# Performance work log

Hardware: AMD Instinct MI355X
Metric: run time of the kernel (lower is better)

The kernel has to match this reference:

```python
import jax, jax.numpy as jnp
import numpy as np

EPS = 1e-5  # torch BatchNorm1d default eps


def setup_inputs() -> dict:
    key = jax.random.key(0)
    ks = jax.random.split(key, 8)
    B, H, D, DO = 8192, 8, 512, 256
    return {
        "x_concepts_encoded": jax.random.normal(ks[0], (B, H, D), dtype=jnp.float32),
        "relevance_weights": jax.random.uniform(ks[1], (B, H), dtype=jnp.float32),
        "bn_gamma": jax.random.uniform(ks[2], (D,), dtype=jnp.float32) + 0.5,
        "bn_beta": jax.random.normal(ks[3], (D,), dtype=jnp.float32) * 0.1,
        "bn_mean": jax.random.normal(ks[4], (D,), dtype=jnp.float32) * 0.1,
        "bn_var": jax.random.uniform(ks[5], (D,), dtype=jnp.float32) + 0.5,
        "W": jax.random.normal(ks[6], (DO, D), dtype=jnp.float32) / np.sqrt(D),
        "b": jax.random.normal(ks[7], (DO,), dtype=jnp.float32) * 0.01,
    }


def reference(x_concepts_encoded, relevance_weights, bn_gamma, bn_beta, bn_mean, bn_var, W, b):
    B, H = relevance_weights.shape
    x = x_concepts_encoded.reshape(B * H, -1)            # [B*H, D]
    # BatchNorm1d (inference: running stats) fused as scale/shift
    inv = bn_gamma * jax.lax.rsqrt(bn_var + EPS)
    h = x * inv + (bn_beta - bn_mean * inv)              # [B*H, D]
    # Swish
    h = h * jax.nn.sigmoid(h)
    # Linear
    out = h @ W.T + b                                    # [B*H, DO]
    # relevance-weighted sum over heads
    out = jnp.einsum('bhd,bh->bd', out.reshape(B, H, -1), relevance_weights)
    return out
```

## Files before the change

kernel.cpp:

```cpp
#include <hip/hip_runtime.h>
#include <hip/hip_bf16.h>

#define NB 8192
#define NH 8
#define ND 512
#define NO 256
#define ROWS 16
#define TPB 512

typedef __attribute__((ext_vector_type(8))) short short8;
typedef __attribute__((ext_vector_type(4))) float f32x4;

__device__ __align__(16) ushort g_wb[NO * ND];

__device__ __forceinline__ ushort f2bf(float f) {
    union { float f; unsigned u; } v; v.f = f;
    unsigned u = v.u;
    unsigned r = u + 0x7FFFu + ((u >> 16) & 1u);
    return (ushort)(r >> 16);
}

__global__ __launch_bounds__(256) void wcvt_kernel(const float* __restrict__ W) {
    int i = (blockIdx.x * 256 + threadIdx.x) * 4;
    float4 w = *(const float4*)(W + i);
    ushort4 o;
    o.x = f2bf(w.x); o.y = f2bf(w.y); o.z = f2bf(w.z); o.w = f2bf(w.w);
    *(ushort4*)(g_wb + i) = o;
}

__device__ __forceinline__ float swishf(float h) {
    return h * __builtin_amdgcn_rcpf(1.0f + __expf(-h));
}

__global__ __launch_bounds__(TPB, 4) void fused_kernel(
    const float* __restrict__ x, const float* __restrict__ rw,
    const float* __restrict__ gamma, const float* __restrict__ beta,
    const float* __restrict__ mean, const float* __restrict__ var,
    const float* __restrict__ bias, float* __restrict__ out)
{
    __shared__ __align__(16) ushort yl[ROWS * ND];
    __shared__ float sumw[ROWS];

    const int tid = threadIdx.x;
    const int b0  = blockIdx.x * ROWS;

    const int d4 = tid & 127;
    const int rh = tid >> 7;
    const int d  = d4 * 4;

    float4 g4 = *(const float4*)(gamma + d);
    float4 v4 = *(const float4*)(var   + d);
    float4 be = *(const float4*)(beta  + d);
    float4 me = *(const float4*)(mean  + d);
    const float ix = g4.x * rsqrtf(v4.x + 1e-5f);
    const float iy = g4.y * rsqrtf(v4.y + 1e-5f);
    const float iz = g4.z * rsqrtf(v4.z + 1e-5f);
    const float iw = g4.w * rsqrtf(v4.w + 1e-5f);
    const float ox = be.x - me.x * ix;
    const float oy = be.y - me.y * iy;
    const float oz = be.z - me.z * iz;
    const float ow = be.w - me.w * iw;

    const float* xr = x + (size_t)(b0 + rh) * (NH * ND) + d;
    float4 cur[NH];
    #pragma unroll
    for (int h = 0; h < NH; ++h) cur[h] = *(const float4*)(xr + h * ND);

    #pragma unroll
    for (int it = 0; it < 4; ++it) {
        const int rr = rh + it * 4;
        float4 nxt[NH];
        if (it < 3) {
            const float* xn = xr + (size_t)4 * NH * ND;
            #pragma unroll
            for (int h = 0; h < NH; ++h) nxt[h] = *(const float4*)(xn + h * ND);
        }
        const float* rwr = rw + (b0 + rr) * NH;
        float4 w0 = *(const float4*)(rwr);
        float4 w1 = *(const float4*)(rwr + 4);
        const float whv[NH] = {w0.x, w0.y, w0.z, w0.w, w1.x, w1.y, w1.z, w1.w};

        float ax = 0.f, ay = 0.f, az = 0.f, aw = 0.f;
        #pragma unroll
        for (int h = 0; h < NH; ++h) {
            const float wh = whv[h];
            ax += wh * swishf(cur[h].x * ix + ox);
            ay += wh * swishf(cur[h].y * iy + oy);
            az += wh * swishf(cur[h].z * iz + oz);
            aw += wh * swishf(cur[h].w * iw + ow);
        }
        const int addr = rr * 1024 + ((d * 2) ^ ((rr & 7) << 4));
        ushort4 o;
        o.x = f2bf(ax); o.y = f2bf(ay); o.z = f2bf(az); o.w = f2bf(aw);
        *(ushort4*)((char*)yl + addr) = o;
        if (d4 == 0)
            sumw[rr] = w0.x + w0.y + w0.z + w0.w + w1.x + w1.y + w1.z + w1.w;

        xr += (size_t)4 * NH * ND;
        #pragma unroll
        for (int h = 0; h < NH; ++h) cur[h] = nxt[h];
    }
    __syncthreads();

    const int lane = tid & 63;
    const int wv   = tid >> 6;
    const int n0   = wv * 32;
    const int lr   = lane & 15;
    const int lk   = (lane >> 4) * 8;

    f32x4 acc0 = {0.f, 0.f, 0.f, 0.f};
    f32x4 acc1 = {0.f, 0.f, 0.f, 0.f};

    const char* ylb = (const char*)yl + lr * 1024;
    const int swz = (lr & 7) << 4;

    #pragma unroll
    for (int ks = 0; ks < 16; ++ks) {
        const int k0 = ks * 32;
        const int kb = (k0 + lk) * 2;
        short8 a = *(const short8*)(ylb + (kb ^ swz));
        const ushort* wp = g_wb + (size_t)(n0 + lr) * ND + k0 + lk;
        short8 bf0 = *(const short8*)(wp);
        short8 bf1 = *(const short8*)(wp + 16 * ND);
        acc0 = __builtin_amdgcn_mfma_f32_16x16x32_bf16(a, bf0, acc0, 0, 0, 0);
        acc1 = __builtin_amdgcn_mfma_f32_16x16x32_bf16(a, bf1, acc1, 0, 0, 0);
    }

    const int rbase = (lane >> 4) * 4;
    f32x4 accs[2] = {acc0, acc1};
    #pragma unroll
    for (int nf = 0; nf < 2; ++nf) {
        const int col = n0 + nf * 16 + lr;
        const float bn = bias[col];
        #pragma unroll
        for (int q = 0; q < 4; ++q) {
            const int r = rbase + q;
            out[(size_t)(b0 + r) * NO + col] = accs[nf][q] + bn * sumw[r];
        }
    }
}

extern "C" void kernel_launch(void* const* d_in, const int* in_sizes, int n_in,
                              void* d_out, int out_size, void* d_ws, size_t ws_size,
                              hipStream_t stream) {
    const float* x     = (const float*)d_in[0];
    const float* rw    = (const float*)d_in[1];
    const float* gamma = (const float*)d_in[2];
    const float* beta  = (const float*)d_in[3];
    const float* mean  = (const float*)d_in[4];
    const float* var   = (const float*)d_in[5];
    const float* W     = (const float*)d_in[6];
    const float* bias  = (const float*)d_in[7];
    float* out = (float*)d_out;

    hipLaunchKernelGGL(wcvt_kernel, dim3((NO * ND) / 1024), dim3(256), 0, stream, W);
    hipLaunchKernelGGL(fused_kernel, dim3(NB / ROWS), dim3(512), 0, stream,
                       x, rw, gamma, beta, mean, var, bias, out);
}
```

Measured before the change: 44.54 us.

## Stage x tiles into LDS via async global_load_lds double buffering

Replaces the register-prefetched global loads of x with direct global-to-LDS 16-byte async loads into a two-stage LDS ring buffer, synchronized with vmcnt waits and barriers. Relevance weights are loaded once into LDS and their per-row sums are recomputed in the epilogue. The aim is deeper memory-level parallelism with lower register pressure on this bandwidth-bound stream. In exchange, LDS use grows by 64KB per block and the launch-bounds occupancy hint is removed, which may reduce blocks per CU. Extra barriers per step are also added.

```diff
diff --git a/kernel.cpp b/kernel.cpp
--- a/kernel.cpp
+++ b/kernel.cpp
@@ -7,6 +7,9 @@
 #define NO 256
 #define ROWS 16
 #define TPB 512
+#define SROWS 4
+#define NSTEP 4
+#define STAGE_FLOATS (SROWS * NH * ND)
 
 typedef __attribute__((ext_vector_type(8))) short short8;
 typedef __attribute__((ext_vector_type(4))) float f32x4;
@@ -32,21 +35,31 @@
     return h * __builtin_amdgcn_rcpf(1.0f + __expf(-h));
 }
 
-__global__ __launch_bounds__(TPB, 4) void fused_kernel(
+__device__ __forceinline__ void gl_lds16(const void* g, void* l) {
+    __builtin_amdgcn_global_load_lds(
+        (const __attribute__((address_space(1))) void*)g,
+        (__attribute__((address_space(3))) void*)l, 16, 0, 0);
+}
+
+__global__ __launch_bounds__(TPB) void fused_kernel(
     const float* __restrict__ x, const float* __restrict__ rw,
     const float* __restrict__ gamma, const float* __restrict__ beta,
     const float* __restrict__ mean, const float* __restrict__ var,
     const float* __restrict__ bias, float* __restrict__ out)
 {
+    __shared__ __align__(16) float xs[2][STAGE_FLOATS];
     __shared__ __align__(16) ushort yl[ROWS * ND];
-    __shared__ float sumw[ROWS];
+    __shared__ float rwl[ROWS * NH];
 
     const int tid = threadIdx.x;
     const int b0  = blockIdx.x * ROWS;
 
-    const int d4 = tid & 127;
-    const int rh = tid >> 7;
-    const int d  = d4 * 4;
+    const int d4  = tid & 127;
+    const int row = tid >> 7;
+    const int d   = d4 * 4;
+
+    if (tid < 32)
+        ((float4*)rwl)[tid] = ((const float4*)(rw + (size_t)b0 * NH))[tid];
 
     float4 g4 = *(const float4*)(gamma + d);
     float4 v4 = *(const float4*)(var   + d);
@@ -61,46 +74,58 @@
     const float oz = be.z - me.z * iz;
     const float ow = be.w - me.w * iw;
 
-    const float* xr = x + (size_t)(b0 + rh) * (NH * ND) + d;
-    float4 cur[NH];
-    #pragma unroll
-    for (int h = 0; h < NH; ++h) cur[h] = *(const float4*)(xr + h * ND);
+    __syncthreads();
+
+    const char* xbase = (const char*)(x + (size_t)b0 * (NH * ND));
+    #define STAGE(s, b) do {                                              \
+        const char* _src = xbase + (size_t)(s) * (SROWS * NH * ND * 4);   \
+        char* _dst = (char*)&xs[b][0];                                    \
+        _Pragma("unroll")                                                 \
+        for (int _r = 0; _r < 8; ++_r) {                                  \
+            const int _off = _r * 8192 + tid * 16;                        \
+            gl_lds16(_src + _off, _dst + _off);                           \
+        }                                                                 \
+    } while (0)
+
+    STAGE(0, 0);
+    STAGE(1, 1);
 
     #pragma unroll
-    for (int it = 0; it < 4; ++it) {
-        const int rr = rh + it * 4;
-        float4 nxt[NH];
-        if (it < 3) {
-            const float* xn = xr + (size_t)4 * NH * ND;
-            #pragma unroll
-            for (int h = 0; h < NH; ++h) nxt[h] = *(const float4*)(xn + h * ND);
-        }
-        const float* rwr = rw + (b0 + rr) * NH;
-        float4 w0 = *(const float4*)(rwr);
-        float4 w1 = *(const float4*)(rwr + 4);
-        const float whv[NH] = {w0.x, w0.y, w0.z, w0.w, w1.x, w1.y, w1.z, w1.w};
+    for (int s = 0; s < NSTEP; ++s) {
+        const int cur = s & 1;
+        if (s < NSTEP - 1) asm volatile("s_waitcnt vmcnt(8)" ::: "memory");
+        else               asm volatile("s_waitcnt vmcnt(0)" ::: "memory");
+        __builtin_amdgcn_s_barrier();
+        asm volatile("" ::: "memory");
+
+        const int rr = s * SROWS + row;
+        const float* xr = xs[cur] + row * (NH * ND) + d;
+        float whv[NH];
+        #pragma unroll
+        for (int h = 0; h < NH; ++h) whv[h] = rwl[rr * NH + h];
 
         float ax = 0.f, ay = 0.f, az = 0.f, aw = 0.f;
         #pragma unroll
         for (int h = 0; h < NH; ++h) {
+            float4 xa = *(const float4*)(xr + h * ND);
             const float wh = whv[h];
-            ax += wh * swishf(cur[h].x * ix + ox);
-            ay += wh * swishf(cur[h].y * iy + oy);
-            az += wh * swishf(cur[h].z * iz + oz);
-            aw += wh * swishf(cur[h].w * iw + ow);
+            ax += wh * swishf(xa.x * ix + ox);
+            ay += wh * swishf(xa.y * iy + oy);
+            az += wh * swishf(xa.z * iz + oz);
+            aw += wh * swishf(xa.w * iw + ow);
         }
         const int addr = rr * 1024 + ((d * 2) ^ ((rr & 7) << 4));
         ushort4 o;
         o.x = f2bf(ax); o.y = f2bf(ay); o.z = f2bf(az); o.w = f2bf(aw);
         *(ushort4*)((char*)yl + addr) = o;
-        if (d4 == 0)
-            sumw[rr] = w0.x + w0.y + w0.z + w0.w + w1.x + w1.y + w1.z + w1.w;
 
-        xr += (size_t)4 * NH * ND;
-        #pragma unroll
-        for (int h = 0; h < NH; ++h) cur[h] = nxt[h];
+        asm volatile("s_waitcnt lgkmcnt(0)" ::: "memory");
+        __builtin_amdgcn_s_barrier();
+        asm volatile("" ::: "memory");
+
+        if (s + 2 < NSTEP) STAGE(s + 2, cur);
     }
-    __syncthreads();
+    #undef STAGE
 
     const int lane = tid & 63;
     const int wv   = tid >> 6;
@@ -114,7 +139,7 @@
     const char* ylb = (const char*)yl + lr * 1024;
     const int swz = (lr & 7) << 4;
 
-    #pragma unroll
+    #pragma unroll 4
     for (int ks = 0; ks < 16; ++ks) {
         const int k0 = ks * 32;
         const int kb = (k0 + lk) * 2;
@@ -127,6 +152,13 @@
     }
 
     const int rbase = (lane >> 4) * 4;
+    float sw[4];
+    #pragma unroll
+    for (int q = 0; q < 4; ++q) {
+        const float* rp = rwl + (rbase + q) * NH;
+        sw[q] = ((rp[0] + rp[1]) + (rp[2] + rp[3])) +
+                ((rp[4] + rp[5]) + (rp[6] + rp[7]));
+    }
     f32x4 accs[2] = {acc0, acc1};
     #pragma unroll
     for (int nf = 0; nf < 2; ++nf) {
@@ -135,7 +167,7 @@
         #pragma unroll
         for (int q = 0; q < 4; ++q) {
             const int r = rbase + q;
-            out[(size_t)(b0 + r) * NO + col] = accs[nf][q] + bn * sumw[r];
+            out[(size_t)(b0 + r) * NO + col] = accs[nf][q] + bn * sw[q];
         }
     }
 }
@@ -154,6 +186,6 @@
     float* out = (float*)d_out;
 
     hipLaunchKernelGGL(wcvt_kernel, dim3((NO * ND) / 1024), dim3(256), 0, stream, W);
-    hipLaunchKernelGGL(fused_kernel, dim3(NB / ROWS), dim3(512), 0, stream,
+    hipLaunchKernelGGL(fused_kernel, dim3(NB / ROWS), dim3(TPB), 0, stream,
                        x, rw, gamma, beta, mean, var, bias, out);
 }
```

Result: slower. 55.47 us (+24.6%).

## Split fused swish-reduce and GEMM into two kernels via workspace buffer

Applied to the files above, without the earlier changes.

Splits the single fused kernel in two. The first computes the BN+swish and head-weighted reduction into a bf16 workspace buffer, and the second loads that buffer into LDS and runs the MFMA GEMM with the bias epilogue. The aim is higher occupancy and simpler kernels with better memory-level parallelism in the bandwidth-bound swish stage. The cost is an extra global round trip of the reduced activations (about 8 MB) and an extra launch.

```diff
diff --git a/kernel.cpp b/kernel.cpp
--- a/kernel.cpp
+++ b/kernel.cpp
@@ -5,8 +5,6 @@
 #define NH 8
 #define ND 512
 #define NO 256
-#define ROWS 16
-#define TPB 512
 
 typedef __attribute__((ext_vector_type(8))) short short8;
 typedef __attribute__((ext_vector_type(4))) float f32x4;
@@ -32,21 +30,16 @@
     return h * __builtin_amdgcn_rcpf(1.0f + __expf(-h));
 }
 
-__global__ __launch_bounds__(TPB, 4) void fused_kernel(
+__global__ __launch_bounds__(256) void swish_kernel(
     const float* __restrict__ x, const float* __restrict__ rw,
     const float* __restrict__ gamma, const float* __restrict__ beta,
     const float* __restrict__ mean, const float* __restrict__ var,
-    const float* __restrict__ bias, float* __restrict__ out)
+    ushort* __restrict__ y)
 {
-    __shared__ __align__(16) ushort yl[ROWS * ND];
-    __shared__ float sumw[ROWS];
-
-    const int tid = threadIdx.x;
-    const int b0  = blockIdx.x * ROWS;
-
-    const int d4 = tid & 127;
-    const int rh = tid >> 7;
-    const int d  = d4 * 4;
+    const int tg  = blockIdx.x * 256 + threadIdx.x;
+    const int row = tg >> 7;
+    const int d4  = tg & 127;
+    const int d   = d4 * 4;
 
     float4 g4 = *(const float4*)(gamma + d);
     float4 v4 = *(const float4*)(var   + d);
@@ -61,44 +54,45 @@
     const float oz = be.z - me.z * iz;
     const float ow = be.w - me.w * iw;
 
-    const float* xr = x + (size_t)(b0 + rh) * (NH * ND) + d;
-    float4 cur[NH];
+    const float* xr = x + (size_t)row * (NH * ND) + d;
+    const float4 w0 = *(const float4*)(rw + row * NH);
+    const float4 w1 = *(const float4*)(rw + row * NH + 4);
+    const float whv[NH] = {w0.x, w0.y, w0.z, w0.w, w1.x, w1.y, w1.z, w1.w};
+
+    float ax = 0.f, ay = 0.f, az = 0.f, aw = 0.f;
     #pragma unroll
-    for (int h = 0; h < NH; ++h) cur[h] = *(const float4*)(xr + h * ND);
+    for (int h = 0; h < NH; ++h) {
+        float4 xa = *(const float4*)(xr + h * ND);
+        const float wh = whv[h];
+        ax += wh * swishf(xa.x * ix + ox);
+        ay += wh * swishf(xa.y * iy + oy);
+        az += wh * swishf(xa.z * iz + oz);
+        aw += wh * swishf(xa.w * iw + ow);
+    }
+    ushort4 o;
+    o.x = f2bf(ax); o.y = f2bf(ay); o.z = f2bf(az); o.w = f2bf(aw);
+    *(ushort4*)(y + (size_t)row * ND + d) = o;
+}
 
-    #pragma unroll
-    for (int it = 0; it < 4; ++it) {
-        const int rr = rh + it * 4;
-        float4 nxt[NH];
-        if (it < 3) {
-            const float* xn = xr + (size_t)4 * NH * ND;
-            #pragma unroll
-            for (int h = 0; h < NH; ++h) nxt[h] = *(const float4*)(xn + h * ND);
+__global__ __launch_bounds__(512) void gemm_kernel(
+    const ushort* __restrict__ y, const float* __restrict__ rw,
+    const float* __restrict__ bias, float* __restrict__ out)
+{
+    __shared__ __align__(16) ushort yl[16 * ND];
+
+    const int tid = threadIdx.x;
+    const int b0  = blockIdx.x * 16;
+
+    {
+        const int rr  = tid >> 5;
+        const int o32 = tid & 31;
+        const char* src = (const char*)(y + (size_t)b0 * ND) + rr * 1024 + o32 * 16;
+        #pragma unroll
+        for (int p = 0; p < 2; ++p) {
+            short8 v = *(const short8*)(src + p * 512);
+            const int boff = (p * 512 + o32 * 16) ^ ((rr & 7) << 4);
+            *(short8*)((char*)yl + rr * 1024 + boff) = v;
         }
-        const float* rwr = rw + (b0 + rr) * NH;
-        float4 w0 = *(const float4*)(rwr);
-        float4 w1 = *(const float4*)(rwr + 4);
-        const float whv[NH] = {w0.x, w0.y, w0.z, w0.w, w1.x, w1.y, w1.z, w1.w};
-
-        float ax = 0.f, ay = 0.f, az = 0.f, aw = 0.f;
-        #pragma unroll
-        for (int h = 0; h < NH; ++h) {
-            const float wh = whv[h];
-            ax += wh * swishf(cur[h].x * ix + ox);
-            ay += wh * swishf(cur[h].y * iy + oy);
-            az += wh * swishf(cur[h].z * iz + oz);
-            aw += wh * swishf(cur[h].w * iw + ow);
-        }
-        const int addr = rr * 1024 + ((d * 2) ^ ((rr & 7) << 4));
-        ushort4 o;
-        o.x = f2bf(ax); o.y = f2bf(ay); o.z = f2bf(az); o.w = f2bf(aw);
-        *(ushort4*)((char*)yl + addr) = o;
-        if (d4 == 0)
-            sumw[rr] = w0.x + w0.y + w0.z + w0.w + w1.x + w1.y + w1.z + w1.w;
-
-        xr += (size_t)4 * NH * ND;
-        #pragma unroll
-        for (int h = 0; h < NH; ++h) cur[h] = nxt[h];
     }
     __syncthreads();
 
@@ -114,7 +108,7 @@
     const char* ylb = (const char*)yl + lr * 1024;
     const int swz = (lr & 7) << 4;
 
-    #pragma unroll
+    #pragma unroll 4
     for (int ks = 0; ks < 16; ++ks) {
         const int k0 = ks * 32;
         const int kb = (k0 + lk) * 2;
@@ -127,6 +121,13 @@
     }
 
     const int rbase = (lane >> 4) * 4;
+    float sw[4];
+    #pragma unroll
+    for (int q = 0; q < 4; ++q) {
+        const float4 a = *(const float4*)(rw + (size_t)(b0 + rbase + q) * NH);
+        const float4 b = *(const float4*)(rw + (size_t)(b0 + rbase + q) * NH + 4);
+        sw[q] = ((a.x + a.y) + (a.z + a.w)) + ((b.x + b.y) + (b.z + b.w));
+    }
     f32x4 accs[2] = {acc0, acc1};
     #pragma unroll
     for (int nf = 0; nf < 2; ++nf) {
@@ -135,7 +136,7 @@
         #pragma unroll
         for (int q = 0; q < 4; ++q) {
             const int r = rbase + q;
-            out[(size_t)(b0 + r) * NO + col] = accs[nf][q] + bn * sumw[r];
+            out[(size_t)(b0 + r) * NO + col] = accs[nf][q] + bn * sw[q];
         }
     }
 }
@@ -153,7 +154,11 @@
     const float* bias  = (const float*)d_in[7];
     float* out = (float*)d_out;
 
+    ushort* y = (ushort*)d_ws;
+
     hipLaunchKernelGGL(wcvt_kernel, dim3((NO * ND) / 1024), dim3(256), 0, stream, W);
-    hipLaunchKernelGGL(fused_kernel, dim3(NB / ROWS), dim3(512), 0, stream,
-                       x, rw, gamma, beta, mean, var, bias, out);
+    hipLaunchKernelGGL(swish_kernel, dim3((NB * 128) / 256), dim3(256), 0, stream,
+                       x, rw, gamma, beta, mean, var, y);
+    hipLaunchKernelGGL(gemm_kernel, dim3(NB / 16), dim3(512), 0, stream,
+                       y, rw, bias, out);
 }
```

Result: slower. 50.17 us (+12.6%).

## Double batch rows per block to reuse W fragments across two MFMA row tiles

Applied to the files above, without the earlier changes.

Each block now handles 32 batch rows instead of 16, so every bf16 W fragment loaded from global memory feeds four MFMAs instead of two, halving W traffic per output row. Relevance weights are staged once into shared memory and the per-row weight sums are computed in the epilogue. The explicit register double-buffering of x loads is removed in favour of direct loads inside the loop, and the occupancy hint in launch bounds is dropped. The trade-offs are half as many blocks, more shared memory per block, and less explicit latency hiding on the memory-bound x stream.

```diff
diff --git a/kernel.cpp b/kernel.cpp
--- a/kernel.cpp
+++ b/kernel.cpp
@@ -5,7 +5,7 @@
 #define NH 8
 #define ND 512
 #define NO 256
-#define ROWS 16
+#define ROWS 32
 #define TPB 512
 
 typedef __attribute__((ext_vector_type(8))) short short8;
@@ -32,21 +32,23 @@
     return h * __builtin_amdgcn_rcpf(1.0f + __expf(-h));
 }
 
-__global__ __launch_bounds__(TPB, 4) void fused_kernel(
+__global__ __launch_bounds__(TPB) void fused_kernel(
     const float* __restrict__ x, const float* __restrict__ rw,
     const float* __restrict__ gamma, const float* __restrict__ beta,
     const float* __restrict__ mean, const float* __restrict__ var,
     const float* __restrict__ bias, float* __restrict__ out)
 {
     __shared__ __align__(16) ushort yl[ROWS * ND];
-    __shared__ float sumw[ROWS];
+    __shared__ float rwl[ROWS * NH];
 
     const int tid = threadIdx.x;
     const int b0  = blockIdx.x * ROWS;
+    const int d4  = tid & 127;
+    const int rh  = tid >> 7;
+    const int d   = d4 * 4;
 
-    const int d4 = tid & 127;
-    const int rh = tid >> 7;
-    const int d  = d4 * 4;
+    if (tid < 64)
+        ((float4*)rwl)[tid] = ((const float4*)(rw + (size_t)b0 * NH))[tid];
 
     float4 g4 = *(const float4*)(gamma + d);
     float4 v4 = *(const float4*)(var   + d);
@@ -61,44 +63,30 @@
     const float oz = be.z - me.z * iz;
     const float ow = be.w - me.w * iw;
 
-    const float* xr = x + (size_t)(b0 + rh) * (NH * ND) + d;
-    float4 cur[NH];
-    #pragma unroll
-    for (int h = 0; h < NH; ++h) cur[h] = *(const float4*)(xr + h * ND);
+    __syncthreads();
 
     #pragma unroll
-    for (int it = 0; it < 4; ++it) {
+    for (int it = 0; it < 8; ++it) {
         const int rr = rh + it * 4;
-        float4 nxt[NH];
-        if (it < 3) {
-            const float* xn = xr + (size_t)4 * NH * ND;
-            #pragma unroll
-            for (int h = 0; h < NH; ++h) nxt[h] = *(const float4*)(xn + h * ND);
-        }
-        const float* rwr = rw + (b0 + rr) * NH;
-        float4 w0 = *(const float4*)(rwr);
-        float4 w1 = *(const float4*)(rwr + 4);
+        const float* xr = x + (size_t)(b0 + rr) * (NH * ND) + d;
+        const float4 w0 = ((const float4*)(rwl + rr * NH))[0];
+        const float4 w1 = ((const float4*)(rwl + rr * NH))[1];
         const float whv[NH] = {w0.x, w0.y, w0.z, w0.w, w1.x, w1.y, w1.z, w1.w};
 
         float ax = 0.f, ay = 0.f, az = 0.f, aw = 0.f;
         #pragma unroll
         for (int h = 0; h < NH; ++h) {
+            float4 xa = *(const float4*)(xr + h * ND);
             const float wh = whv[h];
-            ax += wh * swishf(cur[h].x * ix + ox);
-            ay += wh * swishf(cur[h].y * iy + oy);
-            az += wh * swishf(cur[h].z * iz + oz);
-            aw += wh * swishf(cur[h].w * iw + ow);
+            ax += wh * swishf(xa.x * ix + ox);
+            ay += wh * swishf(xa.y * iy + oy);
+            az += wh * swishf(xa.z * iz + oz);
+            aw += wh * swishf(xa.w * iw + ow);
         }
         const int addr = rr * 1024 + ((d * 2) ^ ((rr & 7) << 4));
         ushort4 o;
         o.x = f2bf(ax); o.y = f2bf(ay); o.z = f2bf(az); o.w = f2bf(aw);
         *(ushort4*)((char*)yl + addr) = o;
-        if (d4 == 0)
-            sumw[rr] = w0.x + w0.y + w0.z + w0.w + w1.x + w1.y + w1.z + w1.w;
-
-        xr += (size_t)4 * NH * ND;
-        #pragma unroll
-        for (int h = 0; h < NH; ++h) cur[h] = nxt[h];
     }
     __syncthreads();
 
@@ -108,26 +96,41 @@
     const int lr   = lane & 15;
     const int lk   = (lane >> 4) * 8;
 
-    f32x4 acc0 = {0.f, 0.f, 0.f, 0.f};
-    f32x4 acc1 = {0.f, 0.f, 0.f, 0.f};
+    f32x4 acc00 = {0.f,0.f,0.f,0.f};
+    f32x4 acc01 = {0.f,0.f,0.f,0.f};
+    f32x4 acc10 = {0.f,0.f,0.f,0.f};
+    f32x4 acc11 = {0.f,0.f,0.f,0.f};
 
-    const char* ylb = (const char*)yl + lr * 1024;
+    const char* ylb0 = (const char*)yl + lr * 1024;
+    const char* ylb1 = (const char*)yl + (lr + 16) * 1024;
     const int swz = (lr & 7) << 4;
 
     #pragma unroll
     for (int ks = 0; ks < 16; ++ks) {
         const int k0 = ks * 32;
         const int kb = (k0 + lk) * 2;
-        short8 a = *(const short8*)(ylb + (kb ^ swz));
+        short8 a0 = *(const short8*)(ylb0 + (kb ^ swz));
+        short8 a1 = *(const short8*)(ylb1 + (kb ^ swz));
         const ushort* wp = g_wb + (size_t)(n0 + lr) * ND + k0 + lk;
         short8 bf0 = *(const short8*)(wp);
         short8 bf1 = *(const short8*)(wp + 16 * ND);
-        acc0 = __builtin_amdgcn_mfma_f32_16x16x32_bf16(a, bf0, acc0, 0, 0, 0);
-        acc1 = __builtin_amdgcn_mfma_f32_16x16x32_bf16(a, bf1, acc1, 0, 0, 0);
+        acc00 = __builtin_amdgcn_mfma_f32_16x16x32_bf16(a0, bf0, acc00, 0, 0, 0);
+        acc01 = __builtin_amdgcn_mfma_f32_16x16x32_bf16(a0, bf1, acc01, 0, 0, 0);
+        acc10 = __builtin_amdgcn_mfma_f32_16x16x32_bf16(a1, bf0, acc10, 0, 0, 0);
+        acc11 = __builtin_amdgcn_mfma_f32_16x16x32_bf16(a1, bf1, acc11, 0, 0, 0);
     }
 
     const int rbase = (lane >> 4) * 4;
-    f32x4 accs[2] = {acc0, acc1};
+    float sw0[4], sw1[4];
+    #pragma unroll
+    for (int q = 0; q < 4; ++q) {
+        const float* rp0 = rwl + (rbase + q) * NH;
+        const float* rp1 = rwl + (16 + rbase + q) * NH;
+        sw0[q] = ((rp0[0]+rp0[1]) + (rp0[2]+rp0[3])) + ((rp0[4]+rp0[5]) + (rp0[6]+rp0[7]));
+        sw1[q] = ((rp1[0]+rp1[1]) + (rp1[2]+rp1[3])) + ((rp1[4]+rp1[5]) + (rp1[6]+rp1[7]));
+    }
+    f32x4 accs0[2] = {acc00, acc01};
+    f32x4 accs1[2] = {acc10, acc11};
     #pragma unroll
     for (int nf = 0; nf < 2; ++nf) {
         const int col = n0 + nf * 16 + lr;
@@ -135,7 +138,8 @@
         #pragma unroll
         for (int q = 0; q < 4; ++q) {
             const int r = rbase + q;
-            out[(size_t)(b0 + r) * NO + col] = accs[nf][q] + bn * sumw[r];
+            out[(size_t)(b0 + r) * NO + col]      = accs0[nf][q] + bn * sw0[q];
+            out[(size_t)(b0 + 16 + r) * NO + col] = accs1[nf][q] + bn * sw1[q];
         }
     }
 }
@@ -154,6 +158,6 @@
     float* out = (float*)d_out;
 
     hipLaunchKernelGGL(wcvt_kernel, dim3((NO * ND) / 1024), dim3(256), 0, stream, W);
-    hipLaunchKernelGGL(fused_kernel, dim3(NB / ROWS), dim3(512), 0, stream,
+    hipLaunchKernelGGL(fused_kernel, dim3(NB / ROWS), dim3(TPB), 0, stream,
                        x, rw, gamma, beta, mean, var, bias, out);
 }
```

Result: faster. 38.87 us (-12.7%).
